# Performance work log

Measured on AMD Instinct MI355X. Metric: run time of the kernel, lower is better.

The kernel has to match this reference:

```python
import jax, jax.numpy as jnp
import numpy as np

NPOINT = 1024   # number of sampled centers
NSAMPLE = 32    # neighbors per center
BN_EPS = 1e-5


def setup_inputs() -> dict:
    key = jax.random.key(0)
    ks = jax.random.split(key, 6)
    B, N, C = 8, 4096, 6
    inp = {
        "xyz": jax.random.normal(ks[0], (B, N, 3), jnp.float32),
        "points": jax.random.normal(ks[1], (B, N, C), jnp.float32),
        "W0": jax.random.normal(ks[2], (64, 9), jnp.float32) * 0.1,
        "g0": jnp.ones((64,), jnp.float32),
        "b0": jnp.zeros((64,), jnp.float32),
        "W1": jax.random.normal(ks[3], (64, 64), jnp.float32) * 0.1,
        "g1": jnp.ones((64,), jnp.float32),
        "b1": jnp.zeros((64,), jnp.float32),
        "W2": jax.random.normal(ks[4], (128, 64), jnp.float32) * 0.1,
        "g2": jnp.ones((128,), jnp.float32),
        "b2": jnp.zeros((128,), jnp.float32),
    }
    return inp


def sample_and_group(xyz, points):
    # xyz: [B,N,3], points: [B,N,C]
    B, N, _ = xyz.shape
    stride = N // NPOINT
    new_xyz = xyz[:, ::stride]                      # [B,S,3] deterministic subsample (FPS surrogate)
    # squared pairwise distances via ||a||^2 + ||b||^2 - 2 a.b  -> [B,S,N]
    d = (jnp.sum(new_xyz * new_xyz, -1)[:, :, None]
         + jnp.sum(xyz * xyz, -1)[:, None, :]
         - 2.0 * jnp.einsum('bsd,bnd->bsn', new_xyz, xyz))
    _, idx = jax.lax.top_k(-d, NSAMPLE)             # [B,S,K] KNN indices
    gather = jax.vmap(lambda arr, i: arr[i])        # per-batch gather: [N,C],[S,K] -> [S,K,C]
    g_xyz = gather(xyz, idx) - new_xyz[:, :, None, :]   # relative coords [B,S,K,3]
    g_pts = gather(points, idx)                     # [B,S,K,C]
    new_points = jnp.concatenate([g_xyz, g_pts], -1)    # [B,S,K,3+C]
    return new_xyz, new_points


def mlp_layer(x, W, g, b):
    # Conv2d(1x1, bias=False) == channel contraction; BN2d with batch stats; ReLU
    x = jnp.einsum('bskc,oc->bsko', x, W)
    m = jnp.mean(x, axis=(0, 1, 2))
    v = jnp.var(x, axis=(0, 1, 2))
    x = (x - m) * jax.lax.rsqrt(v + BN_EPS) * g + b
    return jax.nn.relu(x)


def reference(xyz, points, W0, g0, b0, W1, g1, b1, W2, g2, b2):
    new_xyz, x = sample_and_group(xyz, points)      # x: [B,S,K,9]
    x = mlp_layer(x, W0, g0, b0)
    x = mlp_layer(x, W1, g1, b1)
    x = mlp_layer(x, W2, g2, b2)
    new_points = jnp.max(x, axis=2)                 # max-pool over neighbor dim K -> [B,S,128]
    return new_xyz, new_points
```

## Files before the change

### kernel.cpp

```cpp
#include <hip/hip_runtime.h>
#include <float.h>
#include <stdint.h>

#define TOT   262144
#define NPTS  4096
#define KNN   32
#define BN_EPS 1e-5f
#define CAPV  64

typedef _Float16 f16;
typedef _Float16 f16x2 __attribute__((ext_vector_type(2)));
typedef _Float16 f16x4 __attribute__((ext_vector_type(4)));
typedef _Float16 f16x8 __attribute__((ext_vector_type(8)));
typedef float    f32x4 __attribute__((ext_vector_type(4)));

__device__ __forceinline__ unsigned f2ord(float f){
  unsigned u = __float_as_uint(f);
  return u ^ (((unsigned)((int)u >> 31)) | 0x80000000u);
}
__device__ __forceinline__ f16x2 bnrelu2(f16x2 x, f16x2 a, f16x2 c){
  f16x2 r = x*a + c;
  const f16 z = (f16)0.f;
  r[0] = r[0] > z ? r[0] : z;
  r[1] = r[1] > z ? r[1] : z;
  return r;
}

__global__ __launch_bounds__(256) void prep(const float* __restrict__ xyz,
    float4* __restrict__ xyzp){
  int p = blockIdx.x*256 + threadIdx.x;
  float x = xyz[p*3+0], y = xyz[p*3+1], z = xyz[p*3+2];
  xyzp[p] = make_float4(x, y, z, x*x+y*y+z*z);
}

__global__ __launch_bounds__(256) void knn_gather(
    const float4* __restrict__ xyzp, const float* __restrict__ pts,
    f16* __restrict__ grouped, float* __restrict__ out_newxyz){
  __shared__ unsigned skey[4*CAPV];
  __shared__ unsigned short sidx[4*CAPV];
  __shared__ unsigned lcnt[4];
  const int lane = threadIdx.x & 63;
  const int wv   = threadIdx.x >> 6;
  const int q = blockIdx.x*4 + wv;
  const int b = q >> 10, s = q & 1023;
  const float4* xb = xyzp + b*NPTS;
  const float4 Q = xb[s*4];
  const float qx=Q.x, qy=Q.y, qz=Q.z, qq=Q.w;
  if (lane==0){ out_newxyz[q*3]=qx; out_newxyz[q*3+1]=qy; out_newxyz[q*3+2]=qz;
                lcnt[wv]=0; }

  unsigned m = 0xFFFFFFFFu;
  #pragma unroll 8
  for (int j=0;j<64;j++){
    float4 P = xb[j*64+lane];
    float d = (qq+P.w) - 2.f*(qx*P.x+qy*P.y+qz*P.z);
    unsigned k = f2ord(d);
    m = k<m ? k : m;
  }
  unsigned sm = m;
  #pragma unroll
  for (int k=2;k<=64;k<<=1){
    #pragma unroll
    for (int j=k>>1;j>0;j>>=1){
      unsigned o = __shfl_xor(sm, j, 64);
      bool keepmin = (((lane&k)==0) == ((lane&j)==0));
      sm = keepmin ? (sm<o?sm:o) : (sm>o?sm:o);
    }
  }
  const unsigned U = __shfl(sm, 31, 64);

  unsigned* wk = skey + wv*CAPV;
  unsigned short* wi = sidx + wv*CAPV;
  #pragma unroll 4
  for (int j=0;j<64;j++){
    float4 P = xb[j*64+lane];
    float d = (qq+P.w) - 2.f*(qx*P.x+qy*P.y+qz*P.z);
    unsigned k = f2ord(d);
    if (k <= U){
      unsigned p = atomicAdd(&lcnt[wv], 1u);
      if (p < CAPV){ wk[p]=k; wi[p]=(unsigned short)(j*64+lane); }
    }
  }
  int cnt = (int)lcnt[wv];

  const float* fb = pts + (size_t)b*NPTS*6;
  const int ebase = q*KNN;
  int n = -1;

  if (cnt <= CAPV){
    unsigned myk = (lane<cnt) ? wk[lane] : 0xFFFFFFFFu;
    unsigned myi = (lane<cnt) ? wi[lane] : 0u;
    unsigned long long v = (((unsigned long long)myk)<<16) | myi;
    #pragma unroll
    for (int k=2;k<=64;k<<=1){
      #pragma unroll
      for (int j=k>>1;j>0;j>>=1){
        unsigned long long o = __shfl_xor(v, j, 64);
        bool keepmin = (((lane&k)==0) == ((lane&j)==0));
        v = keepmin ? (v<o?v:o) : (v>o?v:o);
      }
    }
    if (lane < KNN) n = (int)(v & 0xffffull);
  } else {
    unsigned V=0;
    for (int bit=31; bit>=0; --bit){
      unsigned X = V | (1u<<bit);
      int c=0;
      for (int j=0;j<64;j++){
        float4 P = xb[j*64+lane];
        float d = (qq+P.w) - 2.f*(qx*P.x+qy*P.y+qz*P.z);
        c += __popcll(__ballot(f2ord(d) < X));
      }
      if (c < KNN) V = X;
    }
    int cnt2=0;
    for (int pass=0; pass<2; ++pass){
      for (int j=0;j<64;j++){
        float4 P = xb[j*64+lane];
        float d = (qq+P.w) - 2.f*(qx*P.x+qy*P.y+qz*P.z);
        unsigned kk = f2ord(d);
        bool sel = pass ? (kk==V) : (kk<V);
        unsigned long long msk = __ballot(sel);
        int pos = cnt2 + __builtin_amdgcn_mbcnt_hi((unsigned)(msk>>32),
                  __builtin_amdgcn_mbcnt_lo((unsigned)(msk & 0xffffffffull), 0));
        if (sel && pos < KNN){
          int nn = j*64+lane, e = ebase+pos;
          grouped[0*TOT+e]=(f16)(P.x-qx); grouped[1*TOT+e]=(f16)(P.y-qy);
          grouped[2*TOT+e]=(f16)(P.z-qz);
          for (int c6=0;c6<6;c6++) grouped[(3+c6)*TOT+e]=(f16)fb[nn*6+c6];
        }
        cnt2 += __popcll(msk);
      }
    }
  }
  if (n >= 0){
    float4 P = xb[n];
    int e = ebase + lane;
    grouped[0*TOT+e]=(f16)(P.x-qx); grouped[1*TOT+e]=(f16)(P.y-qy);
    grouped[2*TOT+e]=(f16)(P.z-qz);
    #pragma unroll
    for (int c6=0;c6<6;c6++) grouped[(3+c6)*TOT+e]=(f16)fb[n*6+c6];
  }
}

__global__ __launch_bounds__(256) void stats0(
    const f16* __restrict__ grouped, float* __restrict__ s0g){
  const int tid = threadIdx.x, lane = tid&63, wv = tid>>6;
  float v[54];
  #pragma unroll
  for (int i=0;i<54;i++) v[i]=0.f;
  #pragma unroll 1
  for (int it=0; it<2; ++it){
    int n = it*(512*256) + blockIdx.x*256 + tid;
    float g[9];
    #pragma unroll
    for (int c=0;c<9;c++) g[c] = (float)grouped[c*TOT+n];
    #pragma unroll
    for (int c=0;c<9;c++) v[c] += g[c];
    int t=9;
    #pragma unroll
    for (int c=0;c<9;c++)
      #pragma unroll
      for (int c2=0;c2<=c;c2++){ v[t] += g[c]*g[c2]; t++; }
  }
  __shared__ float lds[4][54];
  #pragma unroll
  for (int i=0;i<54;i++){
    float r = v[i];
    #pragma unroll
    for (int off=32; off; off>>=1) r += __shfl_xor(r, off, 64);
    if (lane==0) lds[wv][i]=r;
  }
  __syncthreads();
  if (tid < 54) atomicAdd(&s0g[tid], lds[0][tid]+lds[1][tid]+lds[2][tid]+lds[3][tid]);
}

__global__ void finalize0(const float* __restrict__ s0g,
    const float* __restrict__ W0, const float* __restrict__ g0,
    const float* __restrict__ b0, float* __restrict__ ac0,
    const float* __restrict__ W1, const float* __restrict__ W2,
    f16* __restrict__ W0h, f16* __restrict__ W1h, f16* __restrict__ W2h){
  const int tid = threadIdx.x;
  __shared__ float S[54];
  __shared__ float A0s[64];
  if (tid < 54) S[tid] = s0g[tid];
  __syncthreads();
  if (tid < 64){
    float w[9];
    #pragma unroll
    for (int c=0;c<9;c++) w[c]=W0[tid*9+c];
    float m=0.f;
    #pragma unroll
    for (int c=0;c<9;c++) m += w[c]*S[c];
    float e2=0.f; int t=9;
    #pragma unroll
    for (int c=0;c<9;c++)
      #pragma unroll
      for (int c2=0;c2<=c;c2++){
        float x = w[c]*w[c2]*S[t++];
        e2 += (c2==c) ? x : 2.f*x;
      }
    const float inv = 1.f/(float)TOT;
    m *= inv; e2 *= inv;
    float var = e2 - m*m;
    float a = g0[tid]*rsqrtf(var + BN_EPS);
    ac0[tid]    = a;
    ac0[64+tid] = fmaf(-m, a, b0[tid]);
    A0s[tid]    = a;
  }
  __syncthreads();
  for (int i=tid; i<2048; i+=256){
    int o = i>>5, c = i&31;
    W0h[i] = (f16)(c<9 ? A0s[o]*W0[o*9+c] : 0.f);
  }
  for (int i=tid; i<4096; i+=256) W1h[i] = (f16)W1[i];
  for (int i=tid; i<8192; i+=256) W2h[i] = (f16)W2[i];
}

__global__ __launch_bounds__(256) void layer1(
    const f16* __restrict__ grouped, const f16* __restrict__ W0h,
    const f16* __restrict__ W1h, const float* __restrict__ ac0,
    f16* __restrict__ x1h, float* __restrict__ s1g){
  __shared__ f16 hb[4][16][80];
  __shared__ float sred[4][128];
  const int lane = threadIdx.x & 63, wv = threadIdx.x >> 6;
  const int e16 = lane & 15, q = lane >> 4;
  const int base = blockIdx.x*512 + wv*128;

  f16x8 A0[4];
  #pragma unroll
  for (int m=0;m<4;m++) A0[m] = *(const f16x8*)(W0h + (m*16+e16)*32 + q*8);
  f16x8 A1[4][2];
  #pragma unroll
  for (int m=0;m<4;m++)
    #pragma unroll
    for (int s=0;s<2;s++) A1[m][s] = *(const f16x8*)(W1h + (m*16+e16)*64 + s*32 + q*8);
  float c0i[4][4];
  #pragma unroll
  for (int m=0;m<4;m++)
    #pragma unroll
    for (int i=0;i<4;i++) c0i[m][i] = ac0[64 + m*16 + q*4 + i];
  float ssum[16], ssq[16];
  #pragma unroll
  for (int i=0;i<16;i++){ ssum[i]=0.f; ssq[i]=0.f; }

  #pragma unroll 1
  for (int sub=0; sub<8; ++sub){
    int elem = base + sub*16 + e16;
    f16x8 bg = {};
    if (q==0){
      #pragma unroll
      for (int j=0;j<8;j++) bg[j] = grouped[j*TOT + elem];
    } else if (q==1){
      bg[0] = grouped[8*TOT + elem];
    }
    #pragma unroll
    for (int m=0;m<4;m++){
      f32x4 acc = {c0i[m][0], c0i[m][1], c0i[m][2], c0i[m][3]};
      acc = __builtin_amdgcn_mfma_f32_16x16x32_f16(A0[m], bg, acc, 0,0,0);
      f16x4 w;
      w[0]=(f16)fmaxf(acc[0],0.f); w[1]=(f16)fmaxf(acc[1],0.f);
      w[2]=(f16)fmaxf(acc[2],0.f); w[3]=(f16)fmaxf(acc[3],0.f);
      *(f16x4*)(&hb[wv][e16][m*16 + q*4]) = w;
    }
    f32x4 acc2[4];
    #pragma unroll
    for (int m=0;m<4;m++) acc2[m] = (f32x4){0.f,0.f,0.f,0.f};
    #pragma unroll
    for (int s=0;s<2;s++){
      f16x8 bh = *(const f16x8*)(&hb[wv][e16][s*32 + q*8]);
      #pragma unroll
      for (int m=0;m<4;m++)
        acc2[m] = __builtin_amdgcn_mfma_f32_16x16x32_f16(A1[m][s], bh, acc2[m], 0,0,0);
    }
    #pragma unroll
    for (int m=0;m<4;m++){
      f16x4 w;
      #pragma unroll
      for (int i=0;i<4;i++){
        float x = acc2[m][i];
        ssum[m*4+i] += x;
        ssq[m*4+i]  = fmaf(x, x, ssq[m*4+i]);
        w[i] = (f16)x;
      }
      *(f16x4*)(x1h + (size_t)elem*64 + m*16 + q*4) = w;
    }
  }
  #pragma unroll
  for (int t=0;t<16;t++){
    float a = ssum[t], bq = ssq[t];
    #pragma unroll
    for (int off=1; off<16; off<<=1){
      a  += __shfl_xor(a,  off, 64);
      bq += __shfl_xor(bq, off, 64);
    }
    ssum[t]=a; ssq[t]=bq;
  }
  if (e16==0){
    #pragma unroll
    for (int m=0;m<4;m++)
      #pragma unroll
      for (int i=0;i<4;i++){
        int ch = m*16 + q*4 + i;
        sred[wv][ch]    = ssum[m*4+i];
        sred[wv][64+ch] = ssq[m*4+i];
      }
  }
  __syncthreads();
  const int tid = threadIdx.x;
  if (tid < 128){
    float v = sred[0][tid]+sred[1][tid]+sred[2][tid]+sred[3][tid];
    atomicAdd(&s1g[tid], v);
  }
}

__global__ void finalizeS(const float* __restrict__ sums, int nch,
    const float* __restrict__ gg, const float* __restrict__ bb,
    float* __restrict__ ac, f16* __restrict__ ach){
  int t=threadIdx.x;
  if (t<nch){
    const float inv=1.f/(float)TOT;
    float m=sums[t]*inv;
    float v=sums[nch+t]*inv - m*m;
    float a=gg[t]*rsqrtf(v+BN_EPS);
    float c=fmaf(-m,a,bb[t]);
    ac[t]=a; ac[nch+t]=c;
    if (ach){ ach[t]=(f16)a; ach[nch+t]=(f16)c; }
  }
}

__global__ __launch_bounds__(256) void layer2max(const f16* __restrict__ x1h,
    const f16* __restrict__ W2h, const f16* __restrict__ ac1h,
    float* __restrict__ maxbuf, float* __restrict__ s2g){
  const int lane = threadIdx.x & 63, wv = threadIdx.x >> 6;
  const int e16 = lane & 15, q = lane >> 4;
  f16x8 Bw[8][2];
  #pragma unroll
  for (int nt=0;nt<8;nt++)
    #pragma unroll
    for (int s=0;s<2;s++) Bw[nt][s] = *(const f16x8*)(W2h + (nt*16+e16)*64 + s*32 + q*8);
  f16x2 a1p[8], c1p[8];
  #pragma unroll
  for (int s=0;s<2;s++)
    #pragma unroll
    for (int j2=0;j2<4;j2++){
      a1p[s*4+j2] = ((const f16x2*)ac1h)[s*16 + q*4 + j2];
      c1p[s*4+j2] = ((const f16x2*)(ac1h+64))[s*16 + q*4 + j2];
    }
  float ssum[8], ssq[8];
  #pragma unroll
  for (int i=0;i<8;i++){ ssum[i]=0.f; ssq[i]=0.f; }

  #pragma unroll 1
  for (int qq=0; qq<4; ++qq){
    const int qid = blockIdx.x*16 + wv*4 + qq;
    f32x4 acc[8][2];
    #pragma unroll
    for (int nt=0;nt<8;nt++){ acc[nt][0]=(f32x4){0,0,0,0}; acc[nt][1]=(f32x4){0,0,0,0}; }
    #pragma unroll
    for (int mt=0; mt<2; ++mt){
      #pragma unroll
      for (int s=0;s<2;s++){
        f16x8 a = *(const f16x8*)(x1h + (size_t)(qid*32 + mt*16 + e16)*64 + s*32 + q*8);
        f16x2* a2 = (f16x2*)&a;
        #pragma unroll
        for (int j2=0;j2<4;j2++) a2[j2] = bnrelu2(a2[j2], a1p[s*4+j2], c1p[s*4+j2]);
        #pragma unroll
        for (int nt=0;nt<8;nt++)
          acc[nt][mt] = __builtin_amdgcn_mfma_f32_16x16x32_f16(a, Bw[nt][s], acc[nt][mt], 0,0,0);
      }
    }
    float mx[8];
    #pragma unroll
    for (int nt=0;nt<8;nt++){
      f32x4 u = acc[nt][0], v = acc[nt][1];
      float m1 = fmaxf(fmaxf(u[0],u[1]), fmaxf(u[2],u[3]));
      float m2 = fmaxf(fmaxf(v[0],v[1]), fmaxf(v[2],v[3]));
      mx[nt] = fmaxf(m1, m2);
      ssum[nt] += (u[0]+u[1])+(u[2]+u[3]) + (v[0]+v[1])+(v[2]+v[3]);
      float sq = 0.f;
      #pragma unroll
      for (int i=0;i<4;i++){ sq = fmaf(u[i],u[i],sq); sq = fmaf(v[i],v[i],sq); }
      ssq[nt] += sq;
      mx[nt] = fmaxf(mx[nt], __shfl_xor(mx[nt], 16, 64));
      mx[nt] = fmaxf(mx[nt], __shfl_xor(mx[nt], 32, 64));
    }
    if (lane < 16){
      #pragma unroll
      for (int nt=0;nt<8;nt++) maxbuf[(size_t)qid*128 + nt*16 + lane] = mx[nt];
    }
  }
  #pragma unroll
  for (int nt=0;nt<8;nt++){
    ssum[nt] += __shfl_xor(ssum[nt], 16, 64);
    ssum[nt] += __shfl_xor(ssum[nt], 32, 64);
    ssq[nt]  += __shfl_xor(ssq[nt], 16, 64);
    ssq[nt]  += __shfl_xor(ssq[nt], 32, 64);
  }
  __shared__ float lds[4][256];
  if (q==0){
    #pragma unroll
    for (int nt=0;nt<8;nt++){
      lds[wv][nt*16+e16]     = ssum[nt];
      lds[wv][128+nt*16+e16] = ssq[nt];
    }
  }
  __syncthreads();
  const int tid = threadIdx.x;
  float v = lds[0][tid]+lds[1][tid]+lds[2][tid]+lds[3][tid];
  atomicAdd(&s2g[tid], v);
}

__global__ __launch_bounds__(256) void apply2(
    const float* __restrict__ maxbuf, const float* __restrict__ ac2,
    float* __restrict__ outp){
  int i = blockIdx.x*256 + threadIdx.x;
  int o = i & 127;
  outp[i] = fmaxf(fmaf(maxbuf[i], ac2[o], ac2[128+o]), 0.f);
}

extern "C" void kernel_launch(void* const* d_in, const int* in_sizes, int n_in,
                              void* d_out, int out_size, void* d_ws, size_t ws_size,
                              hipStream_t stream){
  const float* xyz = (const float*)d_in[0];
  const float* pts = (const float*)d_in[1];
  const float* W0  = (const float*)d_in[2];
  const float* g0  = (const float*)d_in[3];
  const float* b0  = (const float*)d_in[4];
  const float* W1  = (const float*)d_in[5];
  const float* g1  = (const float*)d_in[6];
  const float* b1  = (const float*)d_in[7];
  const float* W2  = (const float*)d_in[8];
  const float* g2  = (const float*)d_in[9];
  const float* b2  = (const float*)d_in[10];
  float* out = (float*)d_out;

  float* ws      = (float*)d_ws;
  f16*   grouped = (f16*)ws;
  f16*   x1h     = (f16*)(ws + (size_t)5*TOT);
  float* maxbuf  = ws + (size_t)37*TOT;
  float4* xyzp   = (float4*)(ws + (size_t)41*TOT);
  float* basep   = ws + (size_t)41*TOT + 131072;
  f16*   W0h     = (f16*)basep;
  f16*   W1h     = (f16*)(basep + 1024);
  f16*   W2h     = (f16*)(basep + 3072);
  float* s0g     = basep + 7168;
  float* s1g     = s0g + 64;
  float* s2g     = s1g + 128;
  float* ac0     = s2g + 256;
  float* ac1     = ac0 + 128;
  f16*   ac1h    = (f16*)(ac1 + 128);
  float* ac2     = ac1 + 192;

  (void)hipMemsetAsync(s0g, 0, (64+128+256)*sizeof(float), stream);
  prep      <<< 128, 256, 0, stream>>>(xyz, xyzp);
  knn_gather<<<2048, 256, 0, stream>>>(xyzp, pts, grouped, out);
  stats0    <<< 512, 256, 0, stream>>>(grouped, s0g);
  finalize0 <<<   1, 256, 0, stream>>>(s0g, W0, g0, b0, ac0, W1, W2, W0h, W1h, W2h);
  layer1    <<< 512, 256, 0, stream>>>(grouped, W0h, W1h, ac0, x1h, s1g);
  finalizeS <<<   1, 128, 0, stream>>>(s1g,  64, g1, b1, ac1, ac1h);
  layer2max <<< 512, 256, 0, stream>>>(x1h, W2h, ac1h, maxbuf, s2g);
  finalizeS <<<   1, 128, 0, stream>>>(s2g, 128, g2, b2, ac2, (f16*)0);
  apply2    <<<4096, 256, 0, stream>>>(maxbuf, ac2, out + 24576);
}
```

Measured before the change: 222.3 us.

## Recompute layer-1 in layer2 instead of storing x1, batch KNN queries, MFMA stats

The KNN kernel now handles four query centers per wavefront, reusing each point load across queries, and also writes an element-major padded 16-channel f16 copy of the grouped features. Layer-0 statistics are computed as a Gram matrix with MFMA instead of per-thread scalar accumulation. layer1 no longer stores the 64-channel x1 activation, and layer2max recomputes layers 0 and 1 from the grouped features, removing a large global write and read. The small finalize kernels are folded into their consumers. The cost is duplicated layer-0/1 compute, higher register pressure in the KNN kernel, and fewer KNN blocks.

```diff
diff --git a/kernel.cpp b/kernel.cpp
--- a/kernel.cpp
+++ b/kernel.cpp
@@ -14,6 +14,10 @@
 typedef _Float16 f16x8 __attribute__((ext_vector_type(8)));
 typedef float    f32x4 __attribute__((ext_vector_type(4)));
 
+__device__ __forceinline__ int mbcnt64(unsigned long long m){
+  return __builtin_amdgcn_mbcnt_hi((unsigned)(m>>32),
+         __builtin_amdgcn_mbcnt_lo((unsigned)(m & 0xffffffffull), 0));
+}
 __device__ __forceinline__ unsigned f2ord(float f){
   unsigned u = __float_as_uint(f);
   return u ^ (((unsigned)((int)u >> 31)) | 0x80000000u);
@@ -25,6 +29,24 @@
   r[1] = r[1] > z ? r[1] : z;
   return r;
 }
+__device__ __forceinline__ void writeElem(int n, int e, float qx, float qy, float qz,
+    const float4* __restrict__ xb, const float* __restrict__ fb,
+    f16* __restrict__ grouped, f16* __restrict__ g16){
+  float4 P = xb[n];
+  f16 a[16];
+  a[0]=(f16)(P.x-qx); a[1]=(f16)(P.y-qy); a[2]=(f16)(P.z-qz);
+  #pragma unroll
+  for (int c6=0;c6<6;c6++) a[3+c6] = (f16)fb[n*6+c6];
+  #pragma unroll
+  for (int i=9;i<16;i++) a[i]=(f16)0.f;
+  #pragma unroll
+  for (int c=0;c<9;c++) grouped[c*TOT+e] = a[c];
+  f16x8 lo, hi;
+  #pragma unroll
+  for (int i=0;i<8;i++){ lo[i]=a[i]; hi[i]=a[8+i]; }
+  *(f16x8*)(g16 + (size_t)e*16)     = lo;
+  *(f16x8*)(g16 + (size_t)e*16 + 8) = hi;
+}
 
 __global__ __launch_bounds__(256) void prep(const float* __restrict__ xyz,
     float4* __restrict__ xyzp){
@@ -35,173 +57,193 @@
 
 __global__ __launch_bounds__(256) void knn_gather(
     const float4* __restrict__ xyzp, const float* __restrict__ pts,
-    f16* __restrict__ grouped, float* __restrict__ out_newxyz){
-  __shared__ unsigned skey[4*CAPV];
-  __shared__ unsigned short sidx[4*CAPV];
-  __shared__ unsigned lcnt[4];
+    f16* __restrict__ grouped, f16* __restrict__ g16,
+    float* __restrict__ out_newxyz){
+  __shared__ unsigned wkbuf[4][4][CAPV];
+  __shared__ unsigned short wibuf[4][4][CAPV];
+  __shared__ unsigned lcnt[4][4];
   const int lane = threadIdx.x & 63;
   const int wv   = threadIdx.x >> 6;
-  const int q = blockIdx.x*4 + wv;
-  const int b = q >> 10, s = q & 1023;
+  const int q0 = (blockIdx.x*4 + wv)*4;
+  const int b = q0 >> 10, s0 = q0 & 1023;
   const float4* xb = xyzp + b*NPTS;
-  const float4 Q = xb[s*4];
-  const float qx=Q.x, qy=Q.y, qz=Q.z, qq=Q.w;
-  if (lane==0){ out_newxyz[q*3]=qx; out_newxyz[q*3+1]=qy; out_newxyz[q*3+2]=qz;
-                lcnt[wv]=0; }
-
-  unsigned m = 0xFFFFFFFFu;
-  #pragma unroll 8
-  for (int j=0;j<64;j++){
-    float4 P = xb[j*64+lane];
-    float d = (qq+P.w) - 2.f*(qx*P.x+qy*P.y+qz*P.z);
-    unsigned k = f2ord(d);
-    m = k<m ? k : m;
-  }
-  unsigned sm = m;
-  #pragma unroll
-  for (int k=2;k<=64;k<<=1){
-    #pragma unroll
-    for (int j=k>>1;j>0;j>>=1){
-      unsigned o = __shfl_xor(sm, j, 64);
-      bool keepmin = (((lane&k)==0) == ((lane&j)==0));
-      sm = keepmin ? (sm<o?sm:o) : (sm>o?sm:o);
-    }
-  }
-  const unsigned U = __shfl(sm, 31, 64);
-
-  unsigned* wk = skey + wv*CAPV;
-  unsigned short* wi = sidx + wv*CAPV;
+  float qx[4], qy[4], qz[4], qq[4];
+  #pragma unroll
+  for (int t=0;t<4;t++){
+    float4 Q = xb[(s0+t)*4];
+    qx[t]=Q.x; qy[t]=Q.y; qz[t]=Q.z; qq[t]=Q.w;
+  }
+  if (lane < 4) lcnt[wv][lane] = 0;
+  if (lane == 0){
+    #pragma unroll
+    for (int t=0;t<4;t++){
+      out_newxyz[(q0+t)*3+0]=qx[t]; out_newxyz[(q0+t)*3+1]=qy[t];
+      out_newxyz[(q0+t)*3+2]=qz[t];
+    }
+  }
+
+  unsigned mm[4] = {0xFFFFFFFFu,0xFFFFFFFFu,0xFFFFFFFFu,0xFFFFFFFFu};
   #pragma unroll 4
   for (int j=0;j<64;j++){
     float4 P = xb[j*64+lane];
-    float d = (qq+P.w) - 2.f*(qx*P.x+qy*P.y+qz*P.z);
-    unsigned k = f2ord(d);
-    if (k <= U){
-      unsigned p = atomicAdd(&lcnt[wv], 1u);
-      if (p < CAPV){ wk[p]=k; wi[p]=(unsigned short)(j*64+lane); }
-    }
-  }
-  int cnt = (int)lcnt[wv];
+    #pragma unroll
+    for (int t=0;t<4;t++){
+      float d = (qq[t]+P.w) - 2.f*(qx[t]*P.x+qy[t]*P.y+qz[t]*P.z);
+      unsigned k = f2ord(d);
+      mm[t] = k<mm[t] ? k : mm[t];
+    }
+  }
+  unsigned sm[4] = {mm[0],mm[1],mm[2],mm[3]};
+  #pragma unroll
+  for (int k=2;k<=64;k<<=1){
+    #pragma unroll
+    for (int j=k>>1;j>0;j>>=1){
+      bool keepmin = (((lane&k)==0) == ((lane&j)==0));
+      #pragma unroll
+      for (int t=0;t<4;t++){
+        unsigned o = __shfl_xor(sm[t], j, 64);
+        sm[t] = keepmin ? (sm[t]<o?sm[t]:o) : (sm[t]>o?sm[t]:o);
+      }
+    }
+  }
+  unsigned U[4];
+  #pragma unroll
+  for (int t=0;t<4;t++) U[t] = __shfl(sm[t], 31, 64);
+
+  #pragma unroll 2
+  for (int j=0;j<64;j++){
+    float4 P = xb[j*64+lane];
+    #pragma unroll
+    for (int t=0;t<4;t++){
+      float d = (qq[t]+P.w) - 2.f*(qx[t]*P.x+qy[t]*P.y+qz[t]*P.z);
+      unsigned k = f2ord(d);
+      if (k <= U[t]){
+        unsigned p = atomicAdd(&lcnt[wv][t], 1u);
+        if (p < CAPV){ wkbuf[wv][t][p]=k; wibuf[wv][t][p]=(unsigned short)(j*64+lane); }
+      }
+    }
+  }
+  int cnt[4];
+  #pragma unroll
+  for (int t=0;t<4;t++) cnt[t] = (int)lcnt[wv][t];
+
+  unsigned long long v[4];
+  #pragma unroll
+  for (int t=0;t<4;t++){
+    unsigned myk = (lane<cnt[t]) ? wkbuf[wv][t][lane] : 0xFFFFFFFFu;
+    unsigned myi = (lane<cnt[t]) ? wibuf[wv][t][lane] : 0u;
+    v[t] = (((unsigned long long)myk)<<16) | myi;
+  }
+  #pragma unroll
+  for (int k=2;k<=64;k<<=1){
+    #pragma unroll
+    for (int j=k>>1;j>0;j>>=1){
+      bool keepmin = (((lane&k)==0) == ((lane&j)==0));
+      #pragma unroll
+      for (int t=0;t<4;t++){
+        unsigned long long o = __shfl_xor(v[t], j, 64);
+        v[t] = keepmin ? (v[t]<o?v[t]:o) : (v[t]>o?v[t]:o);
+      }
+    }
+  }
 
   const float* fb = pts + (size_t)b*NPTS*6;
-  const int ebase = q*KNN;
-  int n = -1;
-
-  if (cnt <= CAPV){
-    unsigned myk = (lane<cnt) ? wk[lane] : 0xFFFFFFFFu;
-    unsigned myi = (lane<cnt) ? wi[lane] : 0u;
-    unsigned long long v = (((unsigned long long)myk)<<16) | myi;
-    #pragma unroll
-    for (int k=2;k<=64;k<<=1){
-      #pragma unroll
-      for (int j=k>>1;j>0;j>>=1){
-        unsigned long long o = __shfl_xor(v, j, 64);
-        bool keepmin = (((lane&k)==0) == ((lane&j)==0));
-        v = keepmin ? (v<o?v:o) : (v>o?v:o);
-      }
-    }
-    if (lane < KNN) n = (int)(v & 0xffffull);
-  } else {
-    unsigned V=0;
-    for (int bit=31; bit>=0; --bit){
-      unsigned X = V | (1u<<bit);
-      int c=0;
-      for (int j=0;j<64;j++){
-        float4 P = xb[j*64+lane];
-        float d = (qq+P.w) - 2.f*(qx*P.x+qy*P.y+qz*P.z);
-        c += __popcll(__ballot(f2ord(d) < X));
-      }
-      if (c < KNN) V = X;
-    }
-    int cnt2=0;
-    for (int pass=0; pass<2; ++pass){
-      for (int j=0;j<64;j++){
-        float4 P = xb[j*64+lane];
-        float d = (qq+P.w) - 2.f*(qx*P.x+qy*P.y+qz*P.z);
-        unsigned kk = f2ord(d);
-        bool sel = pass ? (kk==V) : (kk<V);
-        unsigned long long msk = __ballot(sel);
-        int pos = cnt2 + __builtin_amdgcn_mbcnt_hi((unsigned)(msk>>32),
-                  __builtin_amdgcn_mbcnt_lo((unsigned)(msk & 0xffffffffull), 0));
-        if (sel && pos < KNN){
-          int nn = j*64+lane, e = ebase+pos;
-          grouped[0*TOT+e]=(f16)(P.x-qx); grouped[1*TOT+e]=(f16)(P.y-qy);
-          grouped[2*TOT+e]=(f16)(P.z-qz);
-          for (int c6=0;c6<6;c6++) grouped[(3+c6)*TOT+e]=(f16)fb[nn*6+c6];
+  #pragma unroll
+  for (int t=0;t<4;t++){
+    const int ebase = (q0+t)*KNN;
+    if (cnt[t] <= CAPV){
+      if (lane < KNN){
+        int n = (int)(v[t] & 0xffffull);
+        writeElem(n, ebase+lane, qx[t],qy[t],qz[t], xb, fb, grouped, g16);
+      }
+    } else {
+      unsigned V=0;
+      for (int bit=31; bit>=0; --bit){
+        unsigned X = V | (1u<<bit);
+        int c=0;
+        for (int j=0;j<64;j++){
+          float4 P = xb[j*64+lane];
+          float d = (qq[t]+P.w) - 2.f*(qx[t]*P.x+qy[t]*P.y+qz[t]*P.z);
+          c += __popcll(__ballot(f2ord(d) < X));
         }
-        cnt2 += __popcll(msk);
-      }
-    }
-  }
-  if (n >= 0){
-    float4 P = xb[n];
-    int e = ebase + lane;
-    grouped[0*TOT+e]=(f16)(P.x-qx); grouped[1*TOT+e]=(f16)(P.y-qy);
-    grouped[2*TOT+e]=(f16)(P.z-qz);
-    #pragma unroll
-    for (int c6=0;c6<6;c6++) grouped[(3+c6)*TOT+e]=(f16)fb[n*6+c6];
-  }
-}
-
-__global__ __launch_bounds__(256) void stats0(
-    const f16* __restrict__ grouped, float* __restrict__ s0g){
-  const int tid = threadIdx.x, lane = tid&63, wv = tid>>6;
-  float v[54];
-  #pragma unroll
-  for (int i=0;i<54;i++) v[i]=0.f;
-  #pragma unroll 1
-  for (int it=0; it<2; ++it){
-    int n = it*(512*256) + blockIdx.x*256 + tid;
-    float g[9];
-    #pragma unroll
-    for (int c=0;c<9;c++) g[c] = (float)grouped[c*TOT+n];
-    #pragma unroll
-    for (int c=0;c<9;c++) v[c] += g[c];
-    int t=9;
-    #pragma unroll
-    for (int c=0;c<9;c++)
-      #pragma unroll
-      for (int c2=0;c2<=c;c2++){ v[t] += g[c]*g[c2]; t++; }
-  }
-  __shared__ float lds[4][54];
-  #pragma unroll
-  for (int i=0;i<54;i++){
-    float r = v[i];
-    #pragma unroll
-    for (int off=32; off; off>>=1) r += __shfl_xor(r, off, 64);
-    if (lane==0) lds[wv][i]=r;
-  }
-  __syncthreads();
-  if (tid < 54) atomicAdd(&s0g[tid], lds[0][tid]+lds[1][tid]+lds[2][tid]+lds[3][tid]);
-}
-
-__global__ void finalize0(const float* __restrict__ s0g,
+        if (c < KNN) V = X;
+      }
+      int cnt2=0;
+      for (int pass=0; pass<2; ++pass){
+        for (int j=0;j<64;j++){
+          float4 P = xb[j*64+lane];
+          float d = (qq[t]+P.w) - 2.f*(qx[t]*P.x+qy[t]*P.y+qz[t]*P.z);
+          unsigned kk = f2ord(d);
+          bool sel = pass ? (kk==V) : (kk<V);
+          unsigned long long msk = __ballot(sel);
+          int pos = cnt2 + mbcnt64(msk);
+          if (sel && pos < KNN)
+            writeElem(j*64+lane, ebase+pos, qx[t],qy[t],qz[t], xb, fb, grouped, g16);
+          cnt2 += __popcll(msk);
+        }
+      }
+    }
+  }
+}
+
+__global__ __launch_bounds__(256) void stats0m(const f16* __restrict__ grouped,
+    float* __restrict__ s0m){
+  const int lane = threadIdx.x & 63, wv = threadIdx.x >> 6;
+  const int c = lane & 15, q = lane >> 4;
+  const int base = (blockIdx.x*4 + wv)*512;
+  f16x8 cfill = {};
+  if (c == 9){
+    #pragma unroll
+    for (int i=0;i<8;i++) cfill[i] = (f16)1.f;
+  }
+  f32x4 acc = {0.f,0.f,0.f,0.f};
+  #pragma unroll 4
+  for (int chunk=0; chunk<16; ++chunk){
+    int e = base + chunk*32 + q*8;
+    f16x8 f = cfill;
+    if (c < 9) f = *(const f16x8*)(grouped + (size_t)c*TOT + e);
+    acc = __builtin_amdgcn_mfma_f32_16x16x32_f16(f, f, acc, 0,0,0);
+  }
+  __shared__ float red[4][16][16];
+  #pragma unroll
+  for (int i=0;i<4;i++) red[wv][q*4+i][c] = acc[i];
+  __syncthreads();
+  const int tid = threadIdx.x;
+  if (tid < 160){
+    int row = tid>>4, col = tid&15;
+    float vv = red[0][row][col]+red[1][row][col]+red[2][row][col]+red[3][row][col];
+    atomicAdd(&s0m[tid], vv);
+  }
+}
+
+__global__ void finalize0(const float* __restrict__ s0m,
     const float* __restrict__ W0, const float* __restrict__ g0,
     const float* __restrict__ b0, float* __restrict__ ac0,
     const float* __restrict__ W1, const float* __restrict__ W2,
     f16* __restrict__ W0h, f16* __restrict__ W1h, f16* __restrict__ W2h){
   const int tid = threadIdx.x;
-  __shared__ float S[54];
+  __shared__ float S[160];
   __shared__ float A0s[64];
-  if (tid < 54) S[tid] = s0g[tid];
+  if (tid < 160) S[tid] = s0m[tid];
   __syncthreads();
   if (tid < 64){
     float w[9];
     #pragma unroll
     for (int c=0;c<9;c++) w[c]=W0[tid*9+c];
+    const float inv = 1.f/(float)TOT;
     float m=0.f;
     #pragma unroll
-    for (int c=0;c<9;c++) m += w[c]*S[c];
-    float e2=0.f; int t=9;
-    #pragma unroll
-    for (int c=0;c<9;c++)
-      #pragma unroll
-      for (int c2=0;c2<=c;c2++){
-        float x = w[c]*w[c2]*S[t++];
-        e2 += (c2==c) ? x : 2.f*x;
-      }
-    const float inv = 1.f/(float)TOT;
-    m *= inv; e2 *= inv;
+    for (int c=0;c<9;c++) m = fmaf(w[c], S[c*16+9], m);
+    m *= inv;
+    float e2=0.f;
+    #pragma unroll
+    for (int c1=0;c1<9;c1++){
+      float t=0.f;
+      #pragma unroll
+      for (int c2=0;c2<9;c2++) t = fmaf(w[c2], S[c1*16+c2], t);
+      e2 = fmaf(w[c1], t, e2);
+    }
+    e2 *= inv;
     float var = e2 - m*m;
     float a = g0[tid]*rsqrtf(var + BN_EPS);
     ac0[tid]    = a;
@@ -217,11 +259,11 @@
   for (int i=tid; i<8192; i+=256) W2h[i] = (f16)W2[i];
 }
 
-__global__ __launch_bounds__(256) void layer1(
-    const f16* __restrict__ grouped, const f16* __restrict__ W0h,
+__global__ __launch_bounds__(256) void layer1s(
+    const f16* __restrict__ g16, const f16* __restrict__ W0h,
     const f16* __restrict__ W1h, const float* __restrict__ ac0,
-    f16* __restrict__ x1h, float* __restrict__ s1g){
-  __shared__ f16 hb[4][16][80];
+    float* __restrict__ s1g){
+  __shared__ f16 hb0[4][16][80];
   __shared__ float sred[4][128];
   const int lane = threadIdx.x & 63, wv = threadIdx.x >> 6;
   const int e16 = lane & 15, q = lane >> 4;
@@ -248,12 +290,7 @@
   for (int sub=0; sub<8; ++sub){
     int elem = base + sub*16 + e16;
     f16x8 bg = {};
-    if (q==0){
-      #pragma unroll
-      for (int j=0;j<8;j++) bg[j] = grouped[j*TOT + elem];
-    } else if (q==1){
-      bg[0] = grouped[8*TOT + elem];
-    }
+    if (q < 2) bg = *(const f16x8*)(g16 + (size_t)elem*16 + q*8);
     #pragma unroll
     for (int m=0;m<4;m++){
       f32x4 acc = {c0i[m][0], c0i[m][1], c0i[m][2], c0i[m][3]};
@@ -261,30 +298,26 @@
       f16x4 w;
       w[0]=(f16)fmaxf(acc[0],0.f); w[1]=(f16)fmaxf(acc[1],0.f);
       w[2]=(f16)fmaxf(acc[2],0.f); w[3]=(f16)fmaxf(acc[3],0.f);
-      *(f16x4*)(&hb[wv][e16][m*16 + q*4]) = w;
+      *(f16x4*)(&hb0[wv][e16][m*16 + q*4]) = w;
     }
     f32x4 acc2[4];
     #pragma unroll
     for (int m=0;m<4;m++) acc2[m] = (f32x4){0.f,0.f,0.f,0.f};
     #pragma unroll
     for (int s=0;s<2;s++){
-      f16x8 bh = *(const f16x8*)(&hb[wv][e16][s*32 + q*8]);
+      f16x8 bh = *(const f16x8*)(&hb0[wv][e16][s*32 + q*8]);
       #pragma unroll
       for (int m=0;m<4;m++)
         acc2[m] = __builtin_amdgcn_mfma_f32_16x16x32_f16(A1[m][s], bh, acc2[m], 0,0,0);
     }
     #pragma unroll
-    for (int m=0;m<4;m++){
-      f16x4 w;
+    for (int m=0;m<4;m++)
       #pragma unroll
       for (int i=0;i<4;i++){
         float x = acc2[m][i];
         ssum[m*4+i] += x;
         ssq[m*4+i]  = fmaf(x, x, ssq[m*4+i]);
-        w[i] = (f16)x;
-      }
-      *(f16x4*)(x1h + (size_t)elem*64 + m*16 + q*4) = w;
-    }
+      }
   }
   #pragma unroll
   for (int t=0;t<16;t++){
@@ -314,38 +347,54 @@
   }
 }
 
-__global__ void finalizeS(const float* __restrict__ sums, int nch,
-    const float* __restrict__ gg, const float* __restrict__ bb,
-    float* __restrict__ ac, f16* __restrict__ ach){
-  int t=threadIdx.x;
-  if (t<nch){
-    const float inv=1.f/(float)TOT;
-    float m=sums[t]*inv;
-    float v=sums[nch+t]*inv - m*m;
-    float a=gg[t]*rsqrtf(v+BN_EPS);
-    float c=fmaf(-m,a,bb[t]);
-    ac[t]=a; ac[nch+t]=c;
-    if (ach){ ach[t]=(f16)a; ach[nch+t]=(f16)c; }
-  }
-}
-
-__global__ __launch_bounds__(256) void layer2max(const f16* __restrict__ x1h,
-    const f16* __restrict__ W2h, const f16* __restrict__ ac1h,
+__global__ __launch_bounds__(256) void layer2max(
+    const f16* __restrict__ g16, const f16* __restrict__ W0h,
+    const f16* __restrict__ W1h, const f16* __restrict__ W2h,
+    const float* __restrict__ ac0, const float* __restrict__ s1g,
+    const float* __restrict__ g1, const float* __restrict__ b1,
     float* __restrict__ maxbuf, float* __restrict__ s2g){
-  const int lane = threadIdx.x & 63, wv = threadIdx.x >> 6;
+  __shared__ f16 hb0[4][16][80];
+  __shared__ f16 hb1[4][16][80];
+  __shared__ f16 ac1s[128];
+  __shared__ float lds[4][256];
+  const int tid = threadIdx.x;
+  const int lane = tid & 63, wv = tid >> 6;
   const int e16 = lane & 15, q = lane >> 4;
+  if (tid < 64){
+    const float inv = 1.f/(float)TOT;
+    float m = s1g[tid]*inv;
+    float vv = s1g[64+tid]*inv - m*m;
+    float a = g1[tid]*rsqrtf(vv + BN_EPS);
+    ac1s[tid]    = (f16)a;
+    ac1s[64+tid] = (f16)fmaf(-m, a, b1[tid]);
+  }
+  __syncthreads();
+
+  f16x8 A0[4];
+  #pragma unroll
+  for (int m=0;m<4;m++) A0[m] = *(const f16x8*)(W0h + (m*16+e16)*32 + q*8);
+  f16x8 A1[4][2];
+  #pragma unroll
+  for (int m=0;m<4;m++)
+    #pragma unroll
+    for (int s=0;s<2;s++) A1[m][s] = *(const f16x8*)(W1h + (m*16+e16)*64 + s*32 + q*8);
   f16x8 Bw[8][2];
   #pragma unroll
   for (int nt=0;nt<8;nt++)
     #pragma unroll
     for (int s=0;s<2;s++) Bw[nt][s] = *(const f16x8*)(W2h + (nt*16+e16)*64 + s*32 + q*8);
+  float c0i[4][4];
+  #pragma unroll
+  for (int m=0;m<4;m++)
+    #pragma unroll
+    for (int i=0;i<4;i++) c0i[m][i] = ac0[64 + m*16 + q*4 + i];
   f16x2 a1p[8], c1p[8];
   #pragma unroll
-  for (int s=0;s<2;s++)
-    #pragma unroll
-    for (int j2=0;j2<4;j2++){
-      a1p[s*4+j2] = ((const f16x2*)ac1h)[s*16 + q*4 + j2];
-      c1p[s*4+j2] = ((const f16x2*)(ac1h+64))[s*16 + q*4 + j2];
+  for (int m=0;m<4;m++)
+    #pragma unroll
+    for (int j2=0;j2<2;j2++){
+      a1p[m*2+j2] = ((const f16x2*)ac1s)[m*8 + q*2 + j2];
+      c1p[m*2+j2] = ((const f16x2*)(ac1s+64))[m*8 + q*2 + j2];
     }
   float ssum[8], ssq[8];
   #pragma unroll
@@ -354,33 +403,59 @@
   #pragma unroll 1
   for (int qq=0; qq<4; ++qq){
     const int qid = blockIdx.x*16 + wv*4 + qq;
-    f32x4 acc[8][2];
-    #pragma unroll
-    for (int nt=0;nt<8;nt++){ acc[nt][0]=(f32x4){0,0,0,0}; acc[nt][1]=(f32x4){0,0,0,0}; }
-    #pragma unroll
+    f32x4 acc3[8][2];
+    #pragma unroll
+    for (int nt=0;nt<8;nt++){ acc3[nt][0]=(f32x4){0,0,0,0}; acc3[nt][1]=(f32x4){0,0,0,0}; }
+    #pragma unroll 1
     for (int mt=0; mt<2; ++mt){
+      int elem = qid*32 + mt*16 + e16;
+      f16x8 bg = {};
+      if (q < 2) bg = *(const f16x8*)(g16 + (size_t)elem*16 + q*8);
+      #pragma unroll
+      for (int m=0;m<4;m++){
+        f32x4 acc = {c0i[m][0], c0i[m][1], c0i[m][2], c0i[m][3]};
+        acc = __builtin_amdgcn_mfma_f32_16x16x32_f16(A0[m], bg, acc, 0,0,0);
+        f16x4 w;
+        w[0]=(f16)fmaxf(acc[0],0.f); w[1]=(f16)fmaxf(acc[1],0.f);
+        w[2]=(f16)fmaxf(acc[2],0.f); w[3]=(f16)fmaxf(acc[3],0.f);
+        *(f16x4*)(&hb0[wv][e16][m*16 + q*4]) = w;
+      }
+      f32x4 acc2[4];
+      #pragma unroll
+      for (int m=0;m<4;m++) acc2[m] = (f32x4){0.f,0.f,0.f,0.f};
       #pragma unroll
       for (int s=0;s<2;s++){
-        f16x8 a = *(const f16x8*)(x1h + (size_t)(qid*32 + mt*16 + e16)*64 + s*32 + q*8);
-        f16x2* a2 = (f16x2*)&a;
+        f16x8 bh = *(const f16x8*)(&hb0[wv][e16][s*32 + q*8]);
         #pragma unroll
-        for (int j2=0;j2<4;j2++) a2[j2] = bnrelu2(a2[j2], a1p[s*4+j2], c1p[s*4+j2]);
+        for (int m=0;m<4;m++)
+          acc2[m] = __builtin_amdgcn_mfma_f32_16x16x32_f16(A1[m][s], bh, acc2[m], 0,0,0);
+      }
+      #pragma unroll
+      for (int m=0;m<4;m++){
+        f16x2 p0 = bnrelu2((f16x2){(f16)acc2[m][0], (f16)acc2[m][1]}, a1p[m*2  ], c1p[m*2  ]);
+        f16x2 p1 = bnrelu2((f16x2){(f16)acc2[m][2], (f16)acc2[m][3]}, a1p[m*2+1], c1p[m*2+1]);
+        f16x4 w; w[0]=p0[0]; w[1]=p0[1]; w[2]=p1[0]; w[3]=p1[1];
+        *(f16x4*)(&hb1[wv][e16][m*16 + q*4]) = w;
+      }
+      #pragma unroll
+      for (int s=0;s<2;s++){
+        f16x8 af = *(const f16x8*)(&hb1[wv][e16][s*32 + q*8]);
         #pragma unroll
         for (int nt=0;nt<8;nt++)
-          acc[nt][mt] = __builtin_amdgcn_mfma_f32_16x16x32_f16(a, Bw[nt][s], acc[nt][mt], 0,0,0);
+          acc3[nt][mt] = __builtin_amdgcn_mfma_f32_16x16x32_f16(af, Bw[nt][s], acc3[nt][mt], 0,0,0);
       }
     }
     float mx[8];
     #pragma unroll
     for (int nt=0;nt<8;nt++){
-      f32x4 u = acc[nt][0], v = acc[nt][1];
+      f32x4 u = acc3[nt][0], vv = acc3[nt][1];
       float m1 = fmaxf(fmaxf(u[0],u[1]), fmaxf(u[2],u[3]));
-      float m2 = fmaxf(fmaxf(v[0],v[1]), fmaxf(v[2],v[3]));
+      float m2 = fmaxf(fmaxf(vv[0],vv[1]), fmaxf(vv[2],vv[3]));
       mx[nt] = fmaxf(m1, m2);
-      ssum[nt] += (u[0]+u[1])+(u[2]+u[3]) + (v[0]+v[1])+(v[2]+v[3]);
+      ssum[nt] += (u[0]+u[1])+(u[2]+u[3]) + (vv[0]+vv[1])+(vv[2]+vv[3]);
       float sq = 0.f;
       #pragma unroll
-      for (int i=0;i<4;i++){ sq = fmaf(u[i],u[i],sq); sq = fmaf(v[i],v[i],sq); }
+      for (int i=0;i<4;i++){ sq = fmaf(u[i],u[i],sq); sq = fmaf(vv[i],vv[i],sq); }
       ssq[nt] += sq;
       mx[nt] = fmaxf(mx[nt], __shfl_xor(mx[nt], 16, 64));
       mx[nt] = fmaxf(mx[nt], __shfl_xor(mx[nt], 32, 64));
@@ -397,7 +472,6 @@
     ssq[nt]  += __shfl_xor(ssq[nt], 16, 64);
     ssq[nt]  += __shfl_xor(ssq[nt], 32, 64);
   }
-  __shared__ float lds[4][256];
   if (q==0){
     #pragma unroll
     for (int nt=0;nt<8;nt++){
@@ -406,17 +480,28 @@
     }
   }
   __syncthreads();
-  const int tid = threadIdx.x;
   float v = lds[0][tid]+lds[1][tid]+lds[2][tid]+lds[3][tid];
   atomicAdd(&s2g[tid], v);
 }
 
 __global__ __launch_bounds__(256) void apply2(
-    const float* __restrict__ maxbuf, const float* __restrict__ ac2,
+    const float* __restrict__ maxbuf, const float* __restrict__ s2g,
+    const float* __restrict__ g2, const float* __restrict__ b2,
     float* __restrict__ outp){
-  int i = blockIdx.x*256 + threadIdx.x;
+  __shared__ float a2s[128], c2s[128];
+  const int tid = threadIdx.x;
+  if (tid < 128){
+    const float inv = 1.f/(float)TOT;
+    float m = s2g[tid]*inv;
+    float v = s2g[128+tid]*inv - m*m;
+    float a = g2[tid]*rsqrtf(v + BN_EPS);
+    a2s[tid] = a;
+    c2s[tid] = fmaf(-m, a, b2[tid]);
+  }
+  __syncthreads();
+  int i = blockIdx.x*256 + tid;
   int o = i & 127;
-  outp[i] = fmaxf(fmaf(maxbuf[i], ac2[o], ac2[128+o]), 0.f);
+  outp[i] = fmaxf(fmaf(maxbuf[i], a2s[o], c2s[o]), 0.f);
 }
 
 extern "C" void kernel_launch(void* const* d_in, const int* in_sizes, int n_in,
@@ -437,29 +522,24 @@
 
   float* ws      = (float*)d_ws;
   f16*   grouped = (f16*)ws;
-  f16*   x1h     = (f16*)(ws + (size_t)5*TOT);
-  float* maxbuf  = ws + (size_t)37*TOT;
-  float4* xyzp   = (float4*)(ws + (size_t)41*TOT);
-  float* basep   = ws + (size_t)41*TOT + 131072;
+  f16*   g16     = (f16*)(ws + (size_t)5*TOT);
+  float* maxbuf  = ws + (size_t)13*TOT;
+  float4* xyzp   = (float4*)(ws + (size_t)17*TOT);
+  float* basep   = ws + (size_t)17*TOT + 131072;
   f16*   W0h     = (f16*)basep;
   f16*   W1h     = (f16*)(basep + 1024);
   f16*   W2h     = (f16*)(basep + 3072);
-  float* s0g     = basep + 7168;
-  float* s1g     = s0g + 64;
+  float* s0m     = basep + 7168;
+  float* s1g     = s0m + 160;
   float* s2g     = s1g + 128;
   float* ac0     = s2g + 256;
-  float* ac1     = ac0 + 128;
-  f16*   ac1h    = (f16*)(ac1 + 128);
-  float* ac2     = ac1 + 192;
-
-  (void)hipMemsetAsync(s0g, 0, (64+128+256)*sizeof(float), stream);
+
+  (void)hipMemsetAsync(s0m, 0, 544*sizeof(float), stream);
   prep      <<< 128, 256, 0, stream>>>(xyz, xyzp);
-  knn_gather<<<2048, 256, 0, stream>>>(xyzp, pts, grouped, out);
-  stats0    <<< 512, 256, 0, stream>>>(grouped, s0g);
-  finalize0 <<<   1, 256, 0, stream>>>(s0g, W0, g0, b0, ac0, W1, W2, W0h, W1h, W2h);
-  layer1    <<< 512, 256, 0, stream>>>(grouped, W0h, W1h, ac0, x1h, s1g);
-  finalizeS <<<   1, 128, 0, stream>>>(s1g,  64, g1, b1, ac1, ac1h);
-  layer2max <<< 512, 256, 0, stream>>>(x1h, W2h, ac1h, maxbuf, s2g);
-  finalizeS <<<   1, 128, 0, stream>>>(s2g, 128, g2, b2, ac2, (f16*)0);
-  apply2    <<<4096, 256, 0, stream>>>(maxbuf, ac2, out + 24576);
-}
+  knn_gather<<< 512, 256, 0, stream>>>(xyzp, pts, grouped, g16, out);
+  stats0m   <<< 128, 256, 0, stream>>>(grouped, s0m);
+  finalize0 <<<   1, 256, 0, stream>>>(s0m, W0, g0, b0, ac0, W1, W2, W0h, W1h, W2h);
+  layer1s   <<< 512, 256, 0, stream>>>(g16, W0h, W1h, ac0, s1g);
+  layer2max <<< 512, 256, 0, stream>>>(g16, W0h, W1h, W2h, ac0, s1g, g1, b1, maxbuf, s2g);
+  apply2    <<<4096, 256, 0, stream>>>(maxbuf, s2g, g2, b2, out + 24576);
+}
```

Result: slower. 243.1 us (+9.3%).
